# Kernel tuning notes

Hardware: AMD Instinct MI355X
Metric: run time of the kernel (lower is better)

## Reference

```python
import jax, jax.numpy as jnp
import numpy as np

V, H, B, S, L = 32000, 1024, 128, 256, 2


def setup_inputs() -> dict:
    key = jax.random.key(0)
    ks = jax.random.split(key, 20)
    p = lambda k, shape: (0.02 * jax.random.normal(k, shape)).astype(jnp.float32)
    return {
        "input_ids": jax.random.randint(ks[0], (B,), 0, V),
        "hidden": jax.random.normal(ks[1], (L, B, H), dtype=jnp.float32),
        "encoder_outputs": jax.random.normal(ks[2], (S, B, H), dtype=jnp.float32),
        "embed_table": p(ks[3], (V, H)),
        "W_attn": p(ks[4], (H, 2 * H)),
        "b_attn": p(ks[5], (H,)),
        "v": p(ks[6], (H,)),
        "w_ih0": p(ks[7], (3 * H, H)), "w_hh0": p(ks[8], (3 * H, H)),
        "b_ih0": p(ks[9], (3 * H,)), "b_hh0": p(ks[10], (3 * H,)),
        "w_ih1": p(ks[11], (3 * H, H)), "w_hh1": p(ks[12], (3 * H, H)),
        "b_ih1": p(ks[13], (3 * H,)), "b_hh1": p(ks[14], (3 * H,)),
        "W_concat": p(ks[15], (H, 2 * H)), "b_concat": p(ks[16], (H,)),
        "W_out": p(ks[17], (V, H)), "b_out": p(ks[18], (V,)),
    }


def gru_cell(x, h, w_ih, w_hh, b_ih, b_hh):
    # PyTorch GRU cell: gates order (r, z, n)
    gi = x @ w_ih.T + b_ih  # [B, 3H]
    gh = h @ w_hh.T + b_hh
    ir, iz, inn = jnp.split(gi, 3, axis=-1)
    hr, hz, hn = jnp.split(gh, 3, axis=-1)
    r = jax.nn.sigmoid(ir + hr)
    z = jax.nn.sigmoid(iz + hz)
    n = jnp.tanh(inn + r * hn)
    return (1.0 - z) * n + z * h


def reference(input_ids, hidden, encoder_outputs, embed_table, W_attn, b_attn, v,
              w_ih0, w_hh0, b_ih0, b_hh0, w_ih1, w_hh1, b_ih1, b_hh1,
              W_concat, b_concat, W_out, b_out):
    # embedding lookup (dropout is identity in eval mode)
    x = embed_table[input_ids]  # [B, H]
    # 2-layer GRU, single time step
    h0 = gru_cell(x, hidden[0], w_ih0, w_hh0, b_ih0, b_hh0)
    h1 = gru_cell(h0, hidden[1], w_ih1, w_hh1, b_ih1, b_hh1)
    rnn_out = h1                                   # [B, H]
    new_hidden = jnp.stack([h0, h1], axis=0)       # [L, B, H]
    # Bahdanau-style scorer: energy = Linear(cat(h, enc)); score = v . energy
    h_b = jnp.broadcast_to(rnn_out[None, :, :], encoder_outputs.shape)  # [S, B, H]
    feats = jnp.concatenate([h_b, encoder_outputs], axis=-1)            # [S, B, 2H]
    energy = jnp.einsum('sbe,he->sbh', feats, W_attn) + b_attn          # [S, B, H]
    scores = jnp.einsum('sbh,h->bs', energy, v)                         # [B, S]
    attn_weights = jax.nn.softmax(scores, axis=1)                       # [B, S]
    # context = attn_weights @ encoder_outputs (bmm)
    context = jnp.einsum('bs,sbh->bh', attn_weights, encoder_outputs)   # [B, H]
    concat_in = jnp.concatenate([rnn_out, context], axis=-1)            # [B, 2H]
    concat_out = jnp.tanh(concat_in @ W_concat.T + b_concat)            # [B, H]
    output = concat_out @ W_out.T + b_out                               # [B, V]
    return (output, new_hidden, attn_weights[:, None, :])
```

## Files before the change

### kernel.cpp

```cpp
#include <hip/hip_runtime.h>
#include <cstdint>
#include <cstddef>

typedef __attribute__((ext_vector_type(4))) float f32x4;
typedef __attribute__((ext_vector_type(8))) __bf16 bf16x8;
typedef __attribute__((ext_vector_type(8))) short short8;

__device__ __forceinline__ unsigned short f2bf(float f) {
  unsigned u = __builtin_bit_cast(unsigned, f);
  u += 0x7FFFu + ((u >> 16) & 1u);
  return (unsigned short)(u >> 16);
}
__device__ __forceinline__ unsigned pack2(float a, float b) {
  return (unsigned)f2bf(a) | ((unsigned)f2bf(b) << 16);
}

__device__ __forceinline__ void async16(const void* g, void* l) {
  __builtin_amdgcn_global_load_lds((const __attribute__((address_space(1))) unsigned int*)g,
                                   (__attribute__((address_space(3))) unsigned int*)l, 16, 0, 0);
}

struct GemmArgs {
  const unsigned short* A;
  const float* W;
  const float* bias;
  float* C;
};

template <int BN, int WAVES_M, int WAVES_N>
__global__ __launch_bounds__(256, 4) void gemm_bt(GemmArgs g0, GemmArgs g1, int lda, int ldw,
                                                  int N, int Kseg, int seg_stride) {
  constexpr int WM = 128 / WAVES_M, WN = BN / WAVES_N;
  constexpr int MT = WM / 16, NT = WN / 16;
  __shared__ unsigned short a_lds[2][128 * 64];
  __shared__ unsigned short w_lds[2][BN * 64];

  const GemmArgs g = (blockIdx.y == 0) ? g0 : g1;
  const int kbase = blockIdx.z * Kseg;
  const int tid = threadIdx.x;
  const int wave = tid >> 6, lane = tid & 63;
  const int quad = lane >> 4, l16 = lane & 15;
  const int n0 = blockIdx.x * BN;
  const int wm = (wave / WAVES_N) * WM, wn = (wave % WAVES_N) * WN;
  const int niter = Kseg >> 6;

  f32x4 wv[2];

  auto stageA = [&](int k0, int buf) {
#pragma unroll
    for (int i = 0; i < 4; ++i) {
      int chunk = (wave * 4 + i) * 64 + lane;
      int r = chunk >> 3;
      int c = (chunk & 7) ^ (r & 7);
      async16(g.A + (size_t)r * lda + (k0 + c * 8), &a_lds[buf][chunk * 8]);
    }
  };
  auto loadW = [&](int k0) {
    if constexpr (BN == 32) {
      const float* p = g.W + (size_t)(n0 + (tid >> 3)) * ldw + k0 + (tid & 7) * 8;
      wv[0] = *(const f32x4*)p;
      wv[1] = *(const f32x4*)(p + 4);
    } else {
      const float* p = g.W + (size_t)(n0 + (tid >> 4)) * ldw + k0 + ((tid >> 1) & 7) * 8 + (tid & 1) * 4;
      wv[0] = *(const f32x4*)p;
    }
  };
  auto writeW = [&](int buf) {
    if constexpr (BN == 32) {
      int wr = tid >> 3, wc = tid & 7;
      uint4 pk{pack2(wv[0].x, wv[0].y), pack2(wv[0].z, wv[0].w),
               pack2(wv[1].x, wv[1].y), pack2(wv[1].z, wv[1].w)};
      *(uint4*)&w_lds[buf][(wr * 8 + (wc ^ (wr & 7))) * 8] = pk;
    } else {
      int wr = tid >> 4, wc = (tid >> 1) & 7, half = tid & 1;
      uint2 pk{pack2(wv[0].x, wv[0].y), pack2(wv[0].z, wv[0].w)};
      *(uint2*)&w_lds[buf][(wr * 8 + (wc ^ (wr & 7))) * 8 + half * 4] = pk;
    }
  };

  f32x4 acc[MT][NT] = {};

  stageA(kbase, 0);
  loadW(kbase);
  writeW(0);
  __syncthreads();

  for (int ki = 0; ki < niter; ++ki) {
    const int cur = ki & 1;
    const bool more = (ki + 1 < niter);
    if (more) {
      stageA(kbase + (ki + 1) * 64, cur ^ 1);
      loadW(kbase + (ki + 1) * 64);
    }
#pragma unroll
    for (int kh = 0; kh < 2; ++kh) {
      const int c = kh * 4 + quad;
      bf16x8 af[MT], wf[NT];
#pragma unroll
      for (int mt = 0; mt < MT; ++mt) {
        int m = wm + mt * 16 + l16;
        af[mt] = __builtin_bit_cast(bf16x8, *(const short8*)&a_lds[cur][(m * 8 + (c ^ (m & 7))) * 8]);
      }
#pragma unroll
      for (int nt = 0; nt < NT; ++nt) {
        int n = wn + nt * 16 + l16;
        wf[nt] = __builtin_bit_cast(bf16x8, *(const short8*)&w_lds[cur][(n * 8 + (c ^ (n & 7))) * 8]);
      }
#pragma unroll
      for (int mt = 0; mt < MT; ++mt)
#pragma unroll
        for (int nt = 0; nt < NT; ++nt)
          acc[mt][nt] = __builtin_amdgcn_mfma_f32_16x16x32_bf16(af[mt], wf[nt], acc[mt][nt], 0, 0, 0);
    }
    if (more) writeW(cur ^ 1);
    __syncthreads();
  }

  float* C = g.C + (size_t)blockIdx.z * seg_stride;
#pragma unroll
  for (int mt = 0; mt < MT; ++mt)
#pragma unroll
    for (int nt = 0; nt < NT; ++nt) {
      int n = n0 + wn + nt * 16 + l16;
      float bv = (blockIdx.z == 0) ? g.bias[n] : 0.f;
#pragma unroll
      for (int r = 0; r < 4; ++r) {
        int m = wm + mt * 16 + quad * 4 + r;
        C[(size_t)m * N + n] = acc[mt][nt][r] + bv;
      }
    }
}

__global__ __launch_bounds__(256) void prep_kernel(const int* __restrict__ ids,
                                                   const float* __restrict__ hidden,
                                                   const float* __restrict__ embed,
                                                   unsigned short* A0, unsigned short* Hh0,
                                                   unsigned short* Hh1) {
  int job = blockIdx.x >> 7, m = blockIdx.x & 127, t = threadIdx.x;
  const float* src;
  unsigned short* dst;
  if (job == 0) { src = embed + (size_t)ids[m] * 1024; dst = A0; }
  else if (job == 1) { src = hidden + (size_t)m * 1024; dst = Hh0; }
  else { src = hidden + 131072 + (size_t)m * 1024; dst = Hh1; }
  f32x4 v = ((const f32x4*)src)[t];
  uint2 pk{pack2(v.x, v.y), pack2(v.z, v.w)};
  *(uint2*)(dst + (size_t)m * 1024 + t * 4) = pk;
}

__global__ __launch_bounds__(256) void u2_kernel(const float* __restrict__ W_attn,
                                                 const float* __restrict__ v,
                                                 float* __restrict__ u2) {
  int eb = blockIdx.x & 3, hc = blockIdx.x >> 2;
  int e = eb * 256 + threadIdx.x;
  float acc = 0.f;
  int h0 = hc * 32;
#pragma unroll 4
  for (int h = h0; h < h0 + 32; ++h) acc += v[h] * W_attn[(size_t)h * 2048 + 1024 + e];
  atomicAdd(u2 + e, acc);
}

__global__ __launch_bounds__(256) void scores_kernel(const float* __restrict__ enc,
                                                     const float* __restrict__ u2,
                                                     float* __restrict__ sct) {
  int wave = threadIdx.x >> 6, lane = threadIdx.x & 63;
  const f32x4* u4 = (const f32x4*)u2;
  f32x4 uv[4];
#pragma unroll
  for (int p = 0; p < 4; ++p) uv[p] = u4[p * 64 + lane];
  int row0 = (blockIdx.x * 4 + wave) * 4;
  const f32x4* base = (const f32x4*)enc;
  f32x4 ev[4][4];
#pragma unroll
  for (int r = 0; r < 4; ++r)
#pragma unroll
    for (int p = 0; p < 4; ++p) ev[r][p] = base[(size_t)(row0 + r) * 256 + p * 64 + lane];
  float a[4];
#pragma unroll
  for (int r = 0; r < 4; ++r) {
    float s = 0.f;
#pragma unroll
    for (int p = 0; p < 4; ++p)
      s += ev[r][p].x * uv[p].x + ev[r][p].y * uv[p].y + ev[r][p].z * uv[p].z + ev[r][p].w * uv[p].w;
    a[r] = s;
  }
#pragma unroll
  for (int r = 0; r < 4; ++r)
#pragma unroll
    for (int off = 32; off > 0; off >>= 1) a[r] += __shfl_down(a[r], off, 64);
  if (lane == 0) {
#pragma unroll
    for (int r = 0; r < 4; ++r) {
      int row = row0 + r;
      sct[(row & 127) * 256 + (row >> 7)] = a[r];
    }
  }
}

__global__ __launch_bounds__(256) void softmax_kernel(const float* __restrict__ sct,
                                                      float* __restrict__ attn) {
  __shared__ float wmax[4], wsum[4];
  int b = blockIdx.x, t = threadIdx.x;
  int wave = t >> 6, lane = t & 63;
  float sc = sct[b * 256 + t];
  float m = sc;
#pragma unroll
  for (int off = 32; off > 0; off >>= 1) m = fmaxf(m, __shfl_xor(m, off, 64));
  if (lane == 0) wmax[wave] = m;
  __syncthreads();
  float m4 = fmaxf(fmaxf(wmax[0], wmax[1]), fmaxf(wmax[2], wmax[3]));
  float e = __expf(sc - m4);
  float s = e;
#pragma unroll
  for (int off = 32; off > 0; off >>= 1) s += __shfl_xor(s, off, 64);
  if (lane == 0) wsum[wave] = s;
  __syncthreads();
  float tot = (wsum[0] + wsum[1]) + (wsum[2] + wsum[3]);
  attn[b * 256 + t] = e / tot;
}

__global__ __launch_bounds__(256) void context_kernel(const float* __restrict__ enc,
                                                      const float* __restrict__ attn,
                                                      unsigned short* __restrict__ catin) {
  __shared__ float sm[256];
  int b = blockIdx.x >> 2, hc = blockIdx.x & 3;
  int t = threadIdx.x;
  sm[t] = attn[b * 256 + t];
  __syncthreads();
  int h = hc * 256 + t;
  const float* ep = enc + (size_t)b * 1024 + h;
  float a[16];
#pragma unroll
  for (int i = 0; i < 16; ++i) a[i] = 0.f;
  for (int s0 = 0; s0 < 256; s0 += 16)
#pragma unroll
    for (int i = 0; i < 16; ++i) a[i] += sm[s0 + i] * ep[(size_t)(s0 + i) * 131072];
  float tot = 0.f;
#pragma unroll
  for (int i = 0; i < 16; ++i) tot += a[i];
  catin[(size_t)b * 2048 + 1024 + h] = f2bf(tot);
}

__global__ __launch_bounds__(256) void gru_gate(const float* __restrict__ gi,
                                                const float* __restrict__ gh,
                                                const float* __restrict__ h_prev,
                                                float* __restrict__ h_out,
                                                unsigned short* __restrict__ h_bf, int bf_ld) {
  constexpr int SEG = 393216;
  int b = blockIdx.x, j = threadIdx.x * 4;
  const float* gib = gi + (size_t)b * 3072;
  const float* ghb = gh + (size_t)b * 3072;
  f32x4 ir = *(const f32x4*)(gib + j) + *(const f32x4*)(gib + SEG + j);
  f32x4 iz = *(const f32x4*)(gib + 1024 + j) + *(const f32x4*)(gib + SEG + 1024 + j);
  f32x4 in_ = *(const f32x4*)(gib + 2048 + j) + *(const f32x4*)(gib + SEG + 2048 + j);
  f32x4 hr = *(const f32x4*)(ghb + j) + *(const f32x4*)(ghb + SEG + j);
  f32x4 hz = *(const f32x4*)(ghb + 1024 + j) + *(const f32x4*)(ghb + SEG + 1024 + j);
  f32x4 hn = *(const f32x4*)(ghb + 2048 + j) + *(const f32x4*)(ghb + SEG + 2048 + j);
  f32x4 hp = *(const f32x4*)(h_prev + (size_t)b * 1024 + j);
  f32x4 ho;
#pragma unroll
  for (int c = 0; c < 4; ++c) {
    float r = 1.f / (1.f + __expf(-(ir[c] + hr[c])));
    float z = 1.f / (1.f + __expf(-(iz[c] + hz[c])));
    float n = tanhf(in_[c] + r * hn[c]);
    ho[c] = (1.f - z) * n + z * hp[c];
  }
  *(f32x4*)(h_out + (size_t)b * 1024 + j) = ho;
  uint2 pk{pack2(ho.x, ho.y), pack2(ho.z, ho.w)};
  *(uint2*)(h_bf + (size_t)b * bf_ld + j) = pk;
}

__global__ __launch_bounds__(256) void cat_fix(const float* __restrict__ part,
                                               unsigned short* __restrict__ catbf) {
  int m = blockIdx.x, j = threadIdx.x * 4;
  const float* p = part + (size_t)m * 1024 + j;
  f32x4 s = *(const f32x4*)p + *(const f32x4*)(p + 131072) + *(const f32x4*)(p + 262144) +
            *(const f32x4*)(p + 393216);
  f32x4 o;
#pragma unroll
  for (int c = 0; c < 4; ++c) o[c] = tanhf(s[c]);
  uint2 pk{pack2(o.x, o.y), pack2(o.z, o.w)};
  *(uint2*)(catbf + (size_t)m * 1024 + j) = pk;
}

extern "C" void kernel_launch(void* const* d_in, const int* in_sizes, int n_in,
                              void* d_out_, int out_size, void* d_ws, size_t ws_size,
                              hipStream_t stream) {
  const int* ids = (const int*)d_in[0];
  const float* hidden = (const float*)d_in[1];
  const float* enc = (const float*)d_in[2];
  const float* embed = (const float*)d_in[3];
  const float* W_attn = (const float*)d_in[4];
  const float* v = (const float*)d_in[6];
  const float* w_ih0 = (const float*)d_in[7];
  const float* w_hh0 = (const float*)d_in[8];
  const float* b_ih0 = (const float*)d_in[9];
  const float* b_hh0 = (const float*)d_in[10];
  const float* w_ih1 = (const float*)d_in[11];
  const float* w_hh1 = (const float*)d_in[12];
  const float* b_ih1 = (const float*)d_in[13];
  const float* b_hh1 = (const float*)d_in[14];
  const float* W_cat = (const float*)d_in[15];
  const float* b_cat = (const float*)d_in[16];
  const float* W_out = (const float*)d_in[17];
  const float* b_out = (const float*)d_in[18];

  float* out = (float*)d_out_;
  float* h0 = out + 4096000;
  float* h1 = out + 4227072;
  float* attn = out + 4358144;

  float* ws = (float*)d_ws;
  float* gi = ws;
  float* gh = ws + 786432;
  float* u2 = ws + 1572864;
  float* sct = ws + 1573888;
  float* catp = ws + 1606656;
  unsigned short* bfb = (unsigned short*)(ws + 2130944);
  unsigned short* A0 = bfb;
  unsigned short* Hh0 = bfb + 131072;
  unsigned short* Hh1 = bfb + 262144;
  unsigned short* h0bf = bfb + 393216;
  unsigned short* catin = bfb + 524288;
  unsigned short* catbf = bfb + 786432;

  hipMemsetAsync(u2, 0, 1024 * sizeof(float), stream);
  prep_kernel<<<384, 256, 0, stream>>>(ids, hidden, embed, A0, Hh0, Hh1);
  u2_kernel<<<128, 256, 0, stream>>>(W_attn, v, u2);
  scores_kernel<<<2048, 256, 0, stream>>>(enc, u2, sct);
  softmax_kernel<<<128, 256, 0, stream>>>(sct, attn);
  context_kernel<<<512, 256, 0, stream>>>(enc, attn, catin);

  {
    GemmArgs ai{A0, w_ih0, b_ih0, gi}, ah{Hh0, w_hh0, b_hh0, gh};
    gemm_bt<16, 4, 1><<<dim3(192, 2, 2), 256, 0, stream>>>(ai, ah, 1024, 1024, 3072, 512, 393216);
  }
  gru_gate<<<128, 256, 0, stream>>>(gi, gh, hidden, h0, h0bf, 1024);

  {
    GemmArgs ai{h0bf, w_ih1, b_ih1, gi}, ah{Hh1, w_hh1, b_hh1, gh};
    gemm_bt<16, 4, 1><<<dim3(192, 2, 2), 256, 0, stream>>>(ai, ah, 1024, 1024, 3072, 512, 393216);
  }
  gru_gate<<<128, 256, 0, stream>>>(gi, gh, hidden + 131072, h1, catin, 2048);

  {
    GemmArgs ac{catin, W_cat, b_cat, catp};
    gemm_bt<16, 4, 1><<<dim3(64, 1, 4), 256, 0, stream>>>(ac, ac, 2048, 2048, 1024, 512, 131072);
  }
  cat_fix<<<128, 256, 0, stream>>>(catp, catbf);

  {
    GemmArgs ao{catbf, W_out, b_out, out};
    gemm_bt<32, 2, 2><<<dim3(1000, 1, 1), 256, 0, stream>>>(ao, ao, 1024, 1024, 32000, 1024, 0);
  }
}
```

Baseline: 474.5 us.

## Merge independent attention and GRU stages into shared multi-role launches

Folds prep and u2, GRU0 GEMM and scores, gate0 and softmax, and GRU1 GEMM and context into four combined kernels that pick their role from the block index. This cuts the launch count and lets the memory-bound attention work overlap with the GEMM work on idle compute units. The scores body is also split into two phases to lower register pressure, since it now runs under the GEMM's launch bounds. The cost is shared LDS sizing: the attention blocks now reserve the GEMM's LDS allocation, which can reduce their occupancy.

```diff
diff --git a/kernel.cpp b/kernel.cpp
--- a/kernel.cpp
+++ b/kernel.cpp
@@ -28,19 +28,18 @@
 };
 
 template <int BN, int WAVES_M, int WAVES_N>
-__global__ __launch_bounds__(256, 4) void gemm_bt(GemmArgs g0, GemmArgs g1, int lda, int ldw,
-                                                  int N, int Kseg, int seg_stride) {
+__device__ __forceinline__ void gemm_body(const GemmArgs g, int bx, int bz, int lda, int ldw,
+                                          int N, int Kseg, int seg_stride) {
   constexpr int WM = 128 / WAVES_M, WN = BN / WAVES_N;
   constexpr int MT = WM / 16, NT = WN / 16;
   __shared__ unsigned short a_lds[2][128 * 64];
   __shared__ unsigned short w_lds[2][BN * 64];
 
-  const GemmArgs g = (blockIdx.y == 0) ? g0 : g1;
-  const int kbase = blockIdx.z * Kseg;
+  const int kbase = bz * Kseg;
   const int tid = threadIdx.x;
   const int wave = tid >> 6, lane = tid & 63;
   const int quad = lane >> 4, l16 = lane & 15;
-  const int n0 = blockIdx.x * BN;
+  const int n0 = bx * BN;
   const int wm = (wave / WAVES_N) * WM, wn = (wave % WAVES_N) * WN;
   const int niter = Kseg >> 6;
 
@@ -116,13 +115,13 @@
     __syncthreads();
   }
 
-  float* C = g.C + (size_t)blockIdx.z * seg_stride;
+  float* C = g.C + (size_t)bz * seg_stride;
 #pragma unroll
   for (int mt = 0; mt < MT; ++mt)
 #pragma unroll
     for (int nt = 0; nt < NT; ++nt) {
       int n = n0 + wn + nt * 16 + l16;
-      float bv = (blockIdx.z == 0) ? g.bias[n] : 0.f;
+      float bv = (bz == 0) ? g.bias[n] : 0.f;
 #pragma unroll
       for (int r = 0; r < 4; ++r) {
         int m = wm + mt * 16 + quad * 4 + r;
@@ -131,12 +130,19 @@
     }
 }
 
-__global__ __launch_bounds__(256) void prep_kernel(const int* __restrict__ ids,
-                                                   const float* __restrict__ hidden,
-                                                   const float* __restrict__ embed,
-                                                   unsigned short* A0, unsigned short* Hh0,
-                                                   unsigned short* Hh1) {
-  int job = blockIdx.x >> 7, m = blockIdx.x & 127, t = threadIdx.x;
+template <int BN, int WAVES_M, int WAVES_N>
+__global__ __launch_bounds__(256, 4) void gemm_bt(GemmArgs g0, GemmArgs g1, int lda, int ldw,
+                                                  int N, int Kseg, int seg_stride) {
+  gemm_body<BN, WAVES_M, WAVES_N>((blockIdx.y == 0) ? g0 : g1, blockIdx.x, blockIdx.z,
+                                  lda, ldw, N, Kseg, seg_stride);
+}
+
+__device__ __forceinline__ void prep_body(int b, const int* __restrict__ ids,
+                                          const float* __restrict__ hidden,
+                                          const float* __restrict__ embed,
+                                          unsigned short* A0, unsigned short* Hh0,
+                                          unsigned short* Hh1) {
+  int job = b >> 7, m = b & 127, t = threadIdx.x;
   const float* src;
   unsigned short* dst;
   if (job == 0) { src = embed + (size_t)ids[m] * 1024; dst = A0; }
@@ -147,10 +153,9 @@
   *(uint2*)(dst + (size_t)m * 1024 + t * 4) = pk;
 }
 
-__global__ __launch_bounds__(256) void u2_kernel(const float* __restrict__ W_attn,
-                                                 const float* __restrict__ v,
-                                                 float* __restrict__ u2) {
-  int eb = blockIdx.x & 3, hc = blockIdx.x >> 2;
+__device__ __forceinline__ void u2_body(int b, const float* __restrict__ W_attn,
+                                        const float* __restrict__ v, float* __restrict__ u2) {
+  int eb = b & 3, hc = b >> 2;
   int e = eb * 256 + threadIdx.x;
   float acc = 0.f;
   int h0 = hc * 32;
@@ -159,29 +164,30 @@
   atomicAdd(u2 + e, acc);
 }
 
-__global__ __launch_bounds__(256) void scores_kernel(const float* __restrict__ enc,
-                                                     const float* __restrict__ u2,
-                                                     float* __restrict__ sct) {
+__device__ __forceinline__ void scores_body(int b, const float* __restrict__ enc,
+                                            const float* __restrict__ u2,
+                                            float* __restrict__ sct) {
   int wave = threadIdx.x >> 6, lane = threadIdx.x & 63;
   const f32x4* u4 = (const f32x4*)u2;
-  f32x4 uv[4];
-#pragma unroll
-  for (int p = 0; p < 4; ++p) uv[p] = u4[p * 64 + lane];
-  int row0 = (blockIdx.x * 4 + wave) * 4;
+  int row0 = (b * 4 + wave) * 4;
   const f32x4* base = (const f32x4*)enc;
-  f32x4 ev[4][4];
-#pragma unroll
-  for (int r = 0; r < 4; ++r)
-#pragma unroll
-    for (int p = 0; p < 4; ++p) ev[r][p] = base[(size_t)(row0 + r) * 256 + p * 64 + lane];
-  float a[4];
-#pragma unroll
-  for (int r = 0; r < 4; ++r) {
-    float s = 0.f;
-#pragma unroll
-    for (int p = 0; p < 4; ++p)
-      s += ev[r][p].x * uv[p].x + ev[r][p].y * uv[p].y + ev[r][p].z * uv[p].z + ev[r][p].w * uv[p].w;
-    a[r] = s;
+  float a[4] = {0.f, 0.f, 0.f, 0.f};
+#pragma unroll
+  for (int ph = 0; ph < 2; ++ph) {
+    f32x4 uv[2], ev[4][2];
+#pragma unroll
+    for (int p = 0; p < 2; ++p) uv[p] = u4[(ph * 2 + p) * 64 + lane];
+#pragma unroll
+    for (int r = 0; r < 4; ++r)
+#pragma unroll
+      for (int p = 0; p < 2; ++p)
+        ev[r][p] = base[(size_t)(row0 + r) * 256 + (ph * 2 + p) * 64 + lane];
+#pragma unroll
+    for (int r = 0; r < 4; ++r)
+#pragma unroll
+      for (int p = 0; p < 2; ++p)
+        a[r] += ev[r][p].x * uv[p].x + ev[r][p].y * uv[p].y + ev[r][p].z * uv[p].z +
+                ev[r][p].w * uv[p].w;
   }
 #pragma unroll
   for (int r = 0; r < 4; ++r)
@@ -196,10 +202,10 @@
   }
 }
 
-__global__ __launch_bounds__(256) void softmax_kernel(const float* __restrict__ sct,
-                                                      float* __restrict__ attn) {
+__device__ __forceinline__ void softmax_body(int b, const float* __restrict__ sct,
+                                             float* __restrict__ attn) {
   __shared__ float wmax[4], wsum[4];
-  int b = blockIdx.x, t = threadIdx.x;
+  int t = threadIdx.x;
   int wave = t >> 6, lane = t & 63;
   float sc = sct[b * 256 + t];
   float m = sc;
@@ -218,11 +224,11 @@
   attn[b * 256 + t] = e / tot;
 }
 
-__global__ __launch_bounds__(256) void context_kernel(const float* __restrict__ enc,
-                                                      const float* __restrict__ attn,
-                                                      unsigned short* __restrict__ catin) {
+__device__ __forceinline__ void context_body(int blk, const float* __restrict__ enc,
+                                             const float* __restrict__ attn,
+                                             unsigned short* __restrict__ catin) {
   __shared__ float sm[256];
-  int b = blockIdx.x >> 2, hc = blockIdx.x & 3;
+  int b = blk >> 2, hc = blk & 3;
   int t = threadIdx.x;
   sm[t] = attn[b * 256 + t];
   __syncthreads();
@@ -240,13 +246,13 @@
   catin[(size_t)b * 2048 + 1024 + h] = f2bf(tot);
 }
 
-__global__ __launch_bounds__(256) void gru_gate(const float* __restrict__ gi,
-                                                const float* __restrict__ gh,
-                                                const float* __restrict__ h_prev,
-                                                float* __restrict__ h_out,
-                                                unsigned short* __restrict__ h_bf, int bf_ld) {
+__device__ __forceinline__ void gate_body(int b, const float* __restrict__ gi,
+                                          const float* __restrict__ gh,
+                                          const float* __restrict__ h_prev,
+                                          float* __restrict__ h_out,
+                                          unsigned short* __restrict__ h_bf, int bf_ld) {
   constexpr int SEG = 393216;
-  int b = blockIdx.x, j = threadIdx.x * 4;
+  int j = threadIdx.x * 4;
   const float* gib = gi + (size_t)b * 3072;
   const float* ghb = gh + (size_t)b * 3072;
   f32x4 ir = *(const f32x4*)(gib + j) + *(const f32x4*)(gib + SEG + j);
@@ -269,6 +275,14 @@
   *(uint2*)(h_bf + (size_t)b * bf_ld + j) = pk;
 }
 
+__global__ __launch_bounds__(256) void gru_gate(const float* __restrict__ gi,
+                                                const float* __restrict__ gh,
+                                                const float* __restrict__ h_prev,
+                                                float* __restrict__ h_out,
+                                                unsigned short* __restrict__ h_bf, int bf_ld) {
+  gate_body(blockIdx.x, gi, gh, h_prev, h_out, h_bf, bf_ld);
+}
+
 __global__ __launch_bounds__(256) void cat_fix(const float* __restrict__ part,
                                                unsigned short* __restrict__ catbf) {
   int m = blockIdx.x, j = threadIdx.x * 4;
@@ -280,6 +294,49 @@
   for (int c = 0; c < 4; ++c) o[c] = tanhf(s[c]);
   uint2 pk{pack2(o.x, o.y), pack2(o.z, o.w)};
   *(uint2*)(catbf + (size_t)m * 1024 + j) = pk;
+}
+
+__global__ __launch_bounds__(256) void m0_prep_u2(const int* ids, const float* hidden,
+                                                  const float* embed, unsigned short* A0,
+                                                  unsigned short* Hh0, unsigned short* Hh1,
+                                                  const float* W_attn, const float* v,
+                                                  float* u2) {
+  int b = blockIdx.x;
+  if (b < 384) prep_body(b, ids, hidden, embed, A0, Hh0, Hh1);
+  else u2_body(b - 384, W_attn, v, u2);
+}
+
+__global__ __launch_bounds__(256, 4) void m1_gru0_scores(GemmArgs g0, GemmArgs g1,
+                                                         const float* enc, const float* u2,
+                                                         float* sct) {
+  int b = blockIdx.x;
+  if (b < 768) {
+    int bx = b % 192, by = (b / 192) & 1, bz = b / 384;
+    gemm_body<16, 4, 1>(by ? g1 : g0, bx, bz, 1024, 1024, 3072, 512, 393216);
+  } else {
+    scores_body(b - 768, enc, u2, sct);
+  }
+}
+
+__global__ __launch_bounds__(256) void m2_gate0_softmax(const float* gi, const float* gh,
+                                                        const float* h_prev, float* h_out,
+                                                        unsigned short* h_bf,
+                                                        const float* sct, float* attn) {
+  int b = blockIdx.x;
+  if (b < 128) gate_body(b, gi, gh, h_prev, h_out, h_bf, 1024);
+  else softmax_body(b - 128, sct, attn);
+}
+
+__global__ __launch_bounds__(256, 4) void m3_gru1_context(GemmArgs g0, GemmArgs g1,
+                                                          const float* enc, const float* attn,
+                                                          unsigned short* catin) {
+  int b = blockIdx.x;
+  if (b < 768) {
+    int bx = b % 192, by = (b / 192) & 1, bz = b / 384;
+    gemm_body<16, 4, 1>(by ? g1 : g0, bx, bz, 1024, 1024, 3072, 512, 393216);
+  } else {
+    context_body(b - 768, enc, attn, catin);
+  }
 }
 
 extern "C" void kernel_launch(void* const* d_in, const int* in_sizes, int n_in,
@@ -324,22 +381,20 @@
   unsigned short* catbf = bfb + 786432;
 
   hipMemsetAsync(u2, 0, 1024 * sizeof(float), stream);
-  prep_kernel<<<384, 256, 0, stream>>>(ids, hidden, embed, A0, Hh0, Hh1);
-  u2_kernel<<<128, 256, 0, stream>>>(W_attn, v, u2);
-  scores_kernel<<<2048, 256, 0, stream>>>(enc, u2, sct);
-  softmax_kernel<<<128, 256, 0, stream>>>(sct, attn);
-  context_kernel<<<512, 256, 0, stream>>>(enc, attn, catin);
+  m0_prep_u2<<<512, 256, 0, stream>>>(ids, hidden, embed, A0, Hh0, Hh1, W_attn, v, u2);
 
   {
     GemmArgs ai{A0, w_ih0, b_ih0, gi}, ah{Hh0, w_hh0, b_hh0, gh};
-    gemm_bt<16, 4, 1><<<dim3(192, 2, 2), 256, 0, stream>>>(ai, ah, 1024, 1024, 3072, 512, 393216);
-  }
-  gru_gate<<<128, 256, 0, stream>>>(gi, gh, hidden, h0, h0bf, 1024);
+    m1_gru0_scores<<<2816, 256, 0, stream>>>(ai, ah, enc, u2, sct);
+  }
+
+  m2_gate0_softmax<<<256, 256, 0, stream>>>(gi, gh, hidden, h0, h0bf, sct, attn);
 
   {
     GemmArgs ai{h0bf, w_ih1, b_ih1, gi}, ah{Hh1, w_hh1, b_hh1, gh};
-    gemm_bt<16, 4, 1><<<dim3(192, 2, 2), 256, 0, stream>>>(ai, ah, 1024, 1024, 3072, 512, 393216);
-  }
+    m3_gru1_context<<<1280, 256, 0, stream>>>(ai, ah, enc, attn, catin);
+  }
+
   gru_gate<<<128, 256, 0, stream>>>(gi, gh, hidden + 131072, h1, catin, 2048);
 
   {
```

Measured after the change: 467.2 us. Within noise of the previous version (-1.5%).
